# Performance work log

Hardware: AMD Instinct MI355X
Metric: run time of the kernel (lower is better)

The kernel has to match this reference:

```python
import jax, jax.numpy as jnp
import numpy as np

K = 2  # binary (k-ary) heap-layout tree: children of node j are K*j+1 .. K*j+K

def _levels(N):
    # level of node i in heap layout = floor(log2(i+1)); returns list of index arrays, root level first
    lev = np.floor(np.log2(np.arange(N) + 1)).astype(np.int64)
    depth = int(lev.max()) + 1
    return [np.where(lev == l)[0] for l in range(depth)]

def setup_inputs() -> dict:
    key = jax.random.key(0)
    ks = jax.random.split(key, 9)
    B, N, D = 512, 127, 300
    s = 0.05
    return {
        'x':     jax.random.normal(ks[0], (B, N, D), jnp.float32),
        'Wioux': jax.random.normal(ks[1], (D, 3 * D), jnp.float32) * s,
        'bioux': jax.random.normal(ks[2], (3 * D,), jnp.float32) * s,
        'Wiouh': jax.random.normal(ks[3], (D, 3 * D), jnp.float32) * s,
        'biouh': jax.random.normal(ks[4], (3 * D,), jnp.float32) * s,
        'Wfx':   jax.random.normal(ks[5], (D, D), jnp.float32) * s,
        'bfx':   jax.random.normal(ks[6], (D,), jnp.float32) * s,
        'Wfh':   jax.random.normal(ks[7], (D, D), jnp.float32) * s,
        'bfh':   jax.random.normal(ks[8], (D,), jnp.float32) * s,
    }

def reference(x, Wioux, bioux, Wiouh, biouh, Wfx, bfx, Wfh, bfh):
    # Child-Sum Tree-LSTM, level-synchronous (leaves -> root), batched over B trees.
    B, N, D = x.shape
    levels = _levels(N)
    H = jnp.zeros((B, N, D), x.dtype)
    C = jnp.zeros((B, N, D), x.dtype)
    for idx in reversed(levels):  # process deepest level first
        ch = idx[:, None] * K + 1 + np.arange(K)          # [n, K] child node ids (static)
        valid = jnp.asarray((ch < N), x.dtype)[None, :, :, None]  # [1,n,K,1]
        chc = np.minimum(ch, N - 1)
        ch_h = H[:, chc] * valid                           # [B,n,K,D]; padded children -> 0 (leaf case)
        ch_c = C[:, chc] * valid
        h_sum = ch_h.sum(axis=2)                           # child-sum of hidden states [B,n,D]
        xj = x[:, idx]                                     # [B,n,D]
        iou = xj @ Wioux + bioux + h_sum @ Wiouh + biouh   # [B,n,3D]
        i_g, o_g, u_g = jnp.split(iou, 3, axis=-1)
        i_g = jax.nn.sigmoid(i_g)
        o_g = jax.nn.sigmoid(o_g)
        u_g = jnp.tanh(u_g)
        fx = (xj @ Wfx + bfx)[:, :, None, :]               # broadcast over children
        f = jax.nn.sigmoid(jnp.einsum('bnkd,de->bnke', ch_h, Wfh) + bfh + fx)
        c = i_g * u_g + (f * ch_c).sum(axis=2)             # fc sum; padded ch_c==0
        h = o_g * jnp.tanh(c)
        H = H.at[:, idx].set(h)
        C = C.at[:, idx].set(c)
    return H  # per-node hidden states (contexts); root hidden = H[:, 0]
```

## Files before the change

### kernel.cpp

```cpp
#include <hip/hip_runtime.h>
#include <math.h>

#define DIM 300
#define NNODE 127
#define KP 320
#define BK 32
#define ASTR 40
#define MATSZ (KP*KP)

typedef __attribute__((ext_vector_type(8)))  short bf16x8;
typedef __attribute__((ext_vector_type(16))) float f32x16;

__device__ __forceinline__ unsigned short f2bf(float f){
    unsigned u = __float_as_uint(f);
    u += 0x7fffu + ((u >> 16) & 1u);
    return (unsigned short)(u >> 16);
}
__device__ __forceinline__ float sigf(float v){ return 1.0f/(1.0f+__expf(-v)); }
__device__ __forceinline__ float tanh_(float v){
    float t = __expf(-2.0f*fabsf(v));
    float r = (1.0f - t)/(1.0f + t);
    return v < 0.0f ? -r : r;
}

__global__ void prep_weights(const float* __restrict__ Wioux,
                             const float* __restrict__ Wiouh,
                             const float* __restrict__ Wfx,
                             const float* __restrict__ Wfh,
                             unsigned short* __restrict__ WT)
{
    int k = threadIdx.x;
    int n = blockIdx.x;
    int m = blockIdx.y;
    float v = 0.f;
    if (k < DIM && n < DIM){
        if (m < 3)       v = Wioux[k*(3*DIM) + m*DIM + n];
        else if (m < 6)  v = Wiouh[k*(3*DIM) + (m-3)*DIM + n];
        else if (m == 6) v = Wfx[k*DIM + n];
        else             v = Wfh[k*DIM + n];
    }
    WT[m*MATSZ + n*KP + k] = f2bf(v);
}

__global__ __launch_bounds__(256,2)
void leaf_mfma(const float* __restrict__ x,
               const float* __restrict__ bioux, const float* __restrict__ biouh,
               const unsigned short* __restrict__ WT,
               float* __restrict__ H, float* __restrict__ C)
{
    __shared__ __attribute__((aligned(16))) short lds[(1+3)*64*ASTR];
    short* As = lds;
    short* Bs = lds + 64*ASTR;

    const int t = threadIdx.x;
    const int lane = t & 63, wave = t >> 6;
    const int wm = wave >> 1, wn = wave & 1;
    const int lrow = lane & 31, half = lane >> 5;
    const int rowBase = blockIdx.x * 64;
    const int d0 = blockIdx.y * 64;

    const int sr = t >> 2, sseg = t & 3;
    const float* xrow;
    {
        int grow = rowBase + sr;
        int b = grow >> 6, j = 63 + (grow & 63);
        xrow = x + (b*NNODE + j)*DIM;
    }
    const int bm = t >> 5, bn = t & 31;

    f32x16 accI, accO, accU;
    #pragma unroll
    for (int i = 0; i < 16; i++){ accI[i]=0.f; accO[i]=0.f; accU[i]=0.f; }

    for (int k0 = 0; k0 < KP; k0 += BK){
        {
            int kk0 = k0 + sseg*8;
            bf16x8 px;
            if (kk0 + 8 <= DIM){
                float4 a0 = *(const float4*)(xrow + kk0);
                float4 a1 = *(const float4*)(xrow + kk0 + 4);
                px[0]=f2bf(a0.x); px[1]=f2bf(a0.y); px[2]=f2bf(a0.z); px[3]=f2bf(a0.w);
                px[4]=f2bf(a1.x); px[5]=f2bf(a1.y); px[6]=f2bf(a1.z); px[7]=f2bf(a1.w);
            } else {
                #pragma unroll
                for (int e = 0; e < 8; e++){
                    int k = kk0 + e;
                    px[e] = f2bf(k < DIM ? xrow[k] : 0.f);
                }
            }
            *(bf16x8*)(As + sr*ASTR + sseg*8) = px;
        }
        if (bm < 3){
            const unsigned short* wb = WT + bm*MATSZ + k0;
            #pragma unroll
            for (int h2 = 0; h2 < 2; h2++){
                int nn = bn + 32*h2;
                const unsigned short* src = wb + (d0 + nn)*KP;
                short* dst = Bs + bm*64*ASTR + nn*ASTR;
                *(bf16x8*)(dst)      = *(const bf16x8*)(src);
                *(bf16x8*)(dst + 8)  = *(const bf16x8*)(src + 8);
                *(bf16x8*)(dst + 16) = *(const bf16x8*)(src + 16);
                *(bf16x8*)(dst + 24) = *(const bf16x8*)(src + 24);
            }
        }
        __syncthreads();
        #pragma unroll
        for (int kk = 0; kk < 2; kk++){
            int ao = (wm*32 + lrow)*ASTR + kk*16 + half*8;
            bf16x8 ax = *(const bf16x8*)(As + ao);
            int bo = (wn*32 + lrow)*ASTR + kk*16 + half*8;
            bf16x8 b0 = *(const bf16x8*)(Bs + 0*64*ASTR + bo);
            bf16x8 b1 = *(const bf16x8*)(Bs + 1*64*ASTR + bo);
            bf16x8 b2 = *(const bf16x8*)(Bs + 2*64*ASTR + bo);
            accI = __builtin_amdgcn_mfma_f32_32x32x16_bf16(ax, b0, accI, 0, 0, 0);
            accO = __builtin_amdgcn_mfma_f32_32x32x16_bf16(ax, b1, accO, 0, 0, 0);
            accU = __builtin_amdgcn_mfma_f32_32x32x16_bf16(ax, b2, accU, 0, 0, 0);
        }
        __syncthreads();
    }
    int d = d0 + wn*32 + lrow;
    if (d < DIM){
        float bi  = bioux[d]       + biouh[d];
        float bo_ = bioux[DIM+d]   + biouh[DIM+d];
        float bu  = bioux[2*DIM+d] + biouh[2*DIM+d];
        #pragma unroll
        for (int q = 0; q < 16; q++){
            int grow = rowBase + wm*32 + (q&3) + 8*(q>>2) + 4*half;
            int b = grow >> 6, j = 63 + (grow & 63);
            int obase = (b*NNODE + j)*DIM + d;
            float iv = sigf (accI[q] + bi);
            float ov = sigf (accO[q] + bo_);
            float uv = tanh_(accU[q] + bu);
            float cv = iv*uv;
            C[obase] = cv;
            H[obase] = ov*tanh_(cv);
        }
    }
}

__global__ __launch_bounds__(256,2)
void level_mfma(const float* __restrict__ x,
                const float* __restrict__ bioux, const float* __restrict__ biouh,
                const float* __restrict__ bfx,   const float* __restrict__ bfh,
                const unsigned short* __restrict__ WT,
                float* __restrict__ H, float* __restrict__ C,
                int lo, int lshift)
{
    __shared__ __attribute__((aligned(16))) short lds[(4+8)*64*ASTR];
    short* As = lds;
    short* Bs = lds + 4*64*ASTR;

    const int t = threadIdx.x;
    const int lane = t & 63, wave = t >> 6;
    const int wm = wave >> 1, wn = wave & 1;
    const int lrow = lane & 31, half = lane >> 5;
    const int rowBase = blockIdx.x * 64;
    const int d0 = blockIdx.y * 64;
    const int nmask = (1 << lshift) - 1;

    const int sr = t >> 2, sseg = t & 3;
    const float *xrow, *h0row, *h1row;
    {
        int grow = rowBase + sr;
        int b = grow >> lshift, j = lo + (grow & nmask);
        xrow  = x + (b*NNODE + j)*DIM;
        h0row = H + (b*NNODE + 2*j+1)*DIM;
        h1row = H + (b*NNODE + 2*j+2)*DIM;
    }
    const int bm = t >> 5, bn = t & 31;

    f32x16 accI, accO, accU, accFx, accF0, accF1;
    #pragma unroll
    for (int i = 0; i < 16; i++){
        accI[i]=0.f; accO[i]=0.f; accU[i]=0.f;
        accFx[i]=0.f; accF0[i]=0.f; accF1[i]=0.f;
    }

    for (int k0 = 0; k0 < KP; k0 += BK){
        {
            int kk0 = k0 + sseg*8;
            int aoff = sr*ASTR + sseg*8;
            bf16x8 px;
            if (kk0 + 8 <= DIM){
                float4 a0 = *(const float4*)(xrow + kk0);
                float4 a1 = *(const float4*)(xrow + kk0 + 4);
                px[0]=f2bf(a0.x); px[1]=f2bf(a0.y); px[2]=f2bf(a0.z); px[3]=f2bf(a0.w);
                px[4]=f2bf(a1.x); px[5]=f2bf(a1.y); px[6]=f2bf(a1.z); px[7]=f2bf(a1.w);
            } else {
                #pragma unroll
                for (int e = 0; e < 8; e++){
                    int k = kk0 + e;
                    px[e] = f2bf(k < DIM ? xrow[k] : 0.f);
                }
            }
            *(bf16x8*)(As + aoff) = px;

            float h0v[8], h1v[8];
            if (kk0 + 8 <= DIM){
                float4 b0 = *(const float4*)(h0row + kk0);
                float4 b1 = *(const float4*)(h0row + kk0 + 4);
                float4 c0 = *(const float4*)(h1row + kk0);
                float4 c1 = *(const float4*)(h1row + kk0 + 4);
                h0v[0]=b0.x; h0v[1]=b0.y; h0v[2]=b0.z; h0v[3]=b0.w;
                h0v[4]=b1.x; h0v[5]=b1.y; h0v[6]=b1.z; h0v[7]=b1.w;
                h1v[0]=c0.x; h1v[1]=c0.y; h1v[2]=c0.z; h1v[3]=c0.w;
                h1v[4]=c1.x; h1v[5]=c1.y; h1v[6]=c1.z; h1v[7]=c1.w;
            } else {
                #pragma unroll
                for (int e = 0; e < 8; e++){
                    int k = kk0 + e;
                    bool ok = k < DIM;
                    h0v[e] = ok ? h0row[k] : 0.f;
                    h1v[e] = ok ? h1row[k] : 0.f;
                }
            }
            bf16x8 ph, p0, p1;
            #pragma unroll
            for (int e = 0; e < 8; e++){
                p0[e] = f2bf(h0v[e]);
                p1[e] = f2bf(h1v[e]);
                ph[e] = f2bf(h0v[e] + h1v[e]);
            }
            *(bf16x8*)(As + 1*64*ASTR + aoff) = ph;
            *(bf16x8*)(As + 2*64*ASTR + aoff) = p0;
            *(bf16x8*)(As + 3*64*ASTR + aoff) = p1;
        }
        {
            const unsigned short* wb = WT + bm*MATSZ + k0;
            #pragma unroll
            for (int h2 = 0; h2 < 2; h2++){
                int nn = bn + 32*h2;
                const unsigned short* src = wb + (d0 + nn)*KP;
                short* dst = Bs + bm*64*ASTR + nn*ASTR;
                *(bf16x8*)(dst)      = *(const bf16x8*)(src);
                *(bf16x8*)(dst + 8)  = *(const bf16x8*)(src + 8);
                *(bf16x8*)(dst + 16) = *(const bf16x8*)(src + 16);
                *(bf16x8*)(dst + 24) = *(const bf16x8*)(src + 24);
            }
        }
        __syncthreads();
        #pragma unroll
        for (int kk = 0; kk < 2; kk++){
            int ao = (wm*32 + lrow)*ASTR + kk*16 + half*8;
            bf16x8 ax = *(const bf16x8*)(As + 0*64*ASTR + ao);
            bf16x8 ah = *(const bf16x8*)(As + 1*64*ASTR + ao);
            bf16x8 a0 = *(const bf16x8*)(As + 2*64*ASTR + ao);
            bf16x8 a1 = *(const bf16x8*)(As + 3*64*ASTR + ao);
            int bo = (wn*32 + lrow)*ASTR + kk*16 + half*8;
            bf16x8 b0 = *(const bf16x8*)(Bs + 0*64*ASTR + bo);
            bf16x8 b1 = *(const bf16x8*)(Bs + 1*64*ASTR + bo);
            bf16x8 b2 = *(const bf16x8*)(Bs + 2*64*ASTR + bo);
            bf16x8 b3 = *(const bf16x8*)(Bs + 3*64*ASTR + bo);
            bf16x8 b4 = *(const bf16x8*)(Bs + 4*64*ASTR + bo);
            bf16x8 b5 = *(const bf16x8*)(Bs + 5*64*ASTR + bo);
            bf16x8 b6 = *(const bf16x8*)(Bs + 6*64*ASTR + bo);
            bf16x8 b7 = *(const bf16x8*)(Bs + 7*64*ASTR + bo);
            accI  = __builtin_amdgcn_mfma_f32_32x32x16_bf16(ax, b0, accI , 0, 0, 0);
            accI  = __builtin_amdgcn_mfma_f32_32x32x16_bf16(ah, b3, accI , 0, 0, 0);
            accO  = __builtin_amdgcn_mfma_f32_32x32x16_bf16(ax, b1, accO , 0, 0, 0);
            accO  = __builtin_amdgcn_mfma_f32_32x32x16_bf16(ah, b4, accO , 0, 0, 0);
            accU  = __builtin_amdgcn_mfma_f32_32x32x16_bf16(ax, b2, accU , 0, 0, 0);
            accU  = __builtin_amdgcn_mfma_f32_32x32x16_bf16(ah, b5, accU , 0, 0, 0);
            accFx = __builtin_amdgcn_mfma_f32_32x32x16_bf16(ax, b6, accFx, 0, 0, 0);
            accF0 = __builtin_amdgcn_mfma_f32_32x32x16_bf16(a0, b7, accF0, 0, 0, 0);
            accF1 = __builtin_amdgcn_mfma_f32_32x32x16_bf16(a1, b7, accF1, 0, 0, 0);
        }
        __syncthreads();
    }
    int d = d0 + wn*32 + lrow;
    if (d < DIM){
        float bi  = bioux[d]       + biouh[d];
        float bo_ = bioux[DIM+d]   + biouh[DIM+d];
        float bu  = bioux[2*DIM+d] + biouh[2*DIM+d];
        float bf_ = bfx[d] + bfh[d];
        #pragma unroll
        for (int q = 0; q < 16; q++){
            int grow = rowBase + wm*32 + (q&3) + 8*(q>>2) + 4*half;
            int b = grow >> lshift, j = lo + (grow & nmask);
            int obase = (b*NNODE + j)*DIM + d;
            int c0i = (b*NNODE + 2*j+1)*DIM + d;
            int c1i = (b*NNODE + 2*j+2)*DIM + d;
            float iv = sigf (accI[q] + bi);
            float ov = sigf (accO[q] + bo_);
            float uv = tanh_(accU[q] + bu);
            float f0 = sigf (accFx[q] + accF0[q] + bf_);
            float f1 = sigf (accFx[q] + accF1[q] + bf_);
            float cv = iv*uv + f0*C[c0i] + f1*C[c1i];
            C[obase] = cv;
            H[obase] = ov*tanh_(cv);
        }
    }
}

extern "C" void kernel_launch(void* const* d_in, const int* in_sizes, int n_in,
                              void* d_out, int out_size, void* d_ws, size_t ws_size,
                              hipStream_t stream) {
    const float* x     = (const float*)d_in[0];
    const float* Wioux = (const float*)d_in[1];
    const float* bioux = (const float*)d_in[2];
    const float* Wiouh = (const float*)d_in[3];
    const float* biouh = (const float*)d_in[4];
    const float* Wfx   = (const float*)d_in[5];
    const float* bfx   = (const float*)d_in[6];
    const float* Wfh   = (const float*)d_in[7];
    const float* bfh   = (const float*)d_in[8];
    float* H = (float*)d_out;
    float* C = (float*)d_ws;
    unsigned short* WT = (unsigned short*)((char*)d_ws + 78028800);

    prep_weights<<<dim3(KP, 8), KP, 0, stream>>>(Wioux, Wiouh, Wfx, Wfh, WT);
    leaf_mfma<<<dim3(512, 5), 256, 0, stream>>>(x, bioux, biouh, WT, H, C);
    for (int l = 5; l >= 0; l--){
        level_mfma<<<dim3(8 << l, 5), 256, 0, stream>>>(
            x, bioux, biouh, bfx, bfh, WT, H, C, (1 << l) - 1, l);
    }
}
```

Baseline: 532.0 us.

## Load weight fragments directly from global memory and drop LDS staging of B

```diff
diff --git a/kernel.cpp b/kernel.cpp
--- a/kernel.cpp
+++ b/kernel.cpp
@@ -6,7 +6,7 @@
 #define KP 320
 #define BK 32
 #define ASTR 40
-#define MATSZ (KP*KP)
+#define WROW (8*KP)
 
 typedef __attribute__((ext_vector_type(8)))  short bf16x8;
 typedef __attribute__((ext_vector_type(16))) float f32x16;
@@ -39,18 +39,16 @@
         else if (m == 6) v = Wfx[k*DIM + n];
         else             v = Wfh[k*DIM + n];
     }
-    WT[m*MATSZ + n*KP + k] = f2bf(v);
-}
-
-__global__ __launch_bounds__(256,2)
+    WT[n*WROW + m*KP + k] = f2bf(v);
+}
+
+__global__ __launch_bounds__(256,4)
 void leaf_mfma(const float* __restrict__ x,
                const float* __restrict__ bioux, const float* __restrict__ biouh,
                const unsigned short* __restrict__ WT,
                float* __restrict__ H, float* __restrict__ C)
 {
-    __shared__ __attribute__((aligned(16))) short lds[(1+3)*64*ASTR];
-    short* As = lds;
-    short* Bs = lds + 64*ASTR;
+    __shared__ __attribute__((aligned(16))) short As[64*ASTR];
 
     const int t = threadIdx.x;
     const int lane = t & 63, wave = t >> 6;
@@ -66,7 +64,7 @@
         int b = grow >> 6, j = 63 + (grow & 63);
         xrow = x + (b*NNODE + j)*DIM;
     }
-    const int bm = t >> 5, bn = t & 31;
+    const unsigned short* wrow = WT + (size_t)(d0 + wn*32 + lrow)*WROW;
 
     f32x16 accI, accO, accU;
     #pragma unroll
@@ -90,28 +88,15 @@
             }
             *(bf16x8*)(As + sr*ASTR + sseg*8) = px;
         }
-        if (bm < 3){
-            const unsigned short* wb = WT + bm*MATSZ + k0;
-            #pragma unroll
-            for (int h2 = 0; h2 < 2; h2++){
-                int nn = bn + 32*h2;
-                const unsigned short* src = wb + (d0 + nn)*KP;
-                short* dst = Bs + bm*64*ASTR + nn*ASTR;
-                *(bf16x8*)(dst)      = *(const bf16x8*)(src);
-                *(bf16x8*)(dst + 8)  = *(const bf16x8*)(src + 8);
-                *(bf16x8*)(dst + 16) = *(const bf16x8*)(src + 16);
-                *(bf16x8*)(dst + 24) = *(const bf16x8*)(src + 24);
-            }
-        }
         __syncthreads();
         #pragma unroll
         for (int kk = 0; kk < 2; kk++){
             int ao = (wm*32 + lrow)*ASTR + kk*16 + half*8;
             bf16x8 ax = *(const bf16x8*)(As + ao);
-            int bo = (wn*32 + lrow)*ASTR + kk*16 + half*8;
-            bf16x8 b0 = *(const bf16x8*)(Bs + 0*64*ASTR + bo);
-            bf16x8 b1 = *(const bf16x8*)(Bs + 1*64*ASTR + bo);
-            bf16x8 b2 = *(const bf16x8*)(Bs + 2*64*ASTR + bo);
+            const unsigned short* wk = wrow + k0 + kk*16 + half*8;
+            bf16x8 b0 = *(const bf16x8*)(wk);
+            bf16x8 b1 = *(const bf16x8*)(wk + KP);
+            bf16x8 b2 = *(const bf16x8*)(wk + 2*KP);
             accI = __builtin_amdgcn_mfma_f32_32x32x16_bf16(ax, b0, accI, 0, 0, 0);
             accO = __builtin_amdgcn_mfma_f32_32x32x16_bf16(ax, b1, accO, 0, 0, 0);
             accU = __builtin_amdgcn_mfma_f32_32x32x16_bf16(ax, b2, accU, 0, 0, 0);
@@ -138,7 +123,7 @@
     }
 }
 
-__global__ __launch_bounds__(256,2)
+__global__ __launch_bounds__(256,3)
 void level_mfma(const float* __restrict__ x,
                 const float* __restrict__ bioux, const float* __restrict__ biouh,
                 const float* __restrict__ bfx,   const float* __restrict__ bfh,
@@ -146,9 +131,7 @@
                 float* __restrict__ H, float* __restrict__ C,
                 int lo, int lshift)
 {
-    __shared__ __attribute__((aligned(16))) short lds[(4+8)*64*ASTR];
-    short* As = lds;
-    short* Bs = lds + 4*64*ASTR;
+    __shared__ __attribute__((aligned(16))) short As[4*64*ASTR];
 
     const int t = threadIdx.x;
     const int lane = t & 63, wave = t >> 6;
@@ -167,15 +150,15 @@
         h0row = H + (b*NNODE + 2*j+1)*DIM;
         h1row = H + (b*NNODE + 2*j+2)*DIM;
     }
-    const int bm = t >> 5, bn = t & 31;
-
-    f32x16 accI, accO, accU, accFx, accF0, accF1;
+    const unsigned short* wrow = WT + (size_t)(d0 + wn*32 + lrow)*WROW;
+
+    f32x16 accI, accO, accU, accF0, accF1;
     #pragma unroll
     for (int i = 0; i < 16; i++){
-        accI[i]=0.f; accO[i]=0.f; accU[i]=0.f;
-        accFx[i]=0.f; accF0[i]=0.f; accF1[i]=0.f;
-    }
-
+        accI[i]=0.f; accO[i]=0.f; accU[i]=0.f; accF0[i]=0.f; accF1[i]=0.f;
+    }
+
+    #pragma unroll 1
     for (int k0 = 0; k0 < KP; k0 += BK){
         {
             int kk0 = k0 + sseg*8;
@@ -225,43 +208,31 @@
             *(bf16x8*)(As + 2*64*ASTR + aoff) = p0;
             *(bf16x8*)(As + 3*64*ASTR + aoff) = p1;
         }
-        {
-            const unsigned short* wb = WT + bm*MATSZ + k0;
-            #pragma unroll
-            for (int h2 = 0; h2 < 2; h2++){
-                int nn = bn + 32*h2;
-                const unsigned short* src = wb + (d0 + nn)*KP;
-                short* dst = Bs + bm*64*ASTR + nn*ASTR;
-                *(bf16x8*)(dst)      = *(const bf16x8*)(src);
-                *(bf16x8*)(dst + 8)  = *(const bf16x8*)(src + 8);
-                *(bf16x8*)(dst + 16) = *(const bf16x8*)(src + 16);
-                *(bf16x8*)(dst + 24) = *(const bf16x8*)(src + 24);
-            }
-        }
         __syncthreads();
         #pragma unroll
         for (int kk = 0; kk < 2; kk++){
             int ao = (wm*32 + lrow)*ASTR + kk*16 + half*8;
-            bf16x8 ax = *(const bf16x8*)(As + 0*64*ASTR + ao);
+            const unsigned short* wk = wrow + k0 + kk*16 + half*8;
+            bf16x8 ax = *(const bf16x8*)(As + ao);
+            bf16x8 b0 = *(const bf16x8*)(wk);
+            bf16x8 b1 = *(const bf16x8*)(wk + KP);
+            bf16x8 b2 = *(const bf16x8*)(wk + 2*KP);
+            bf16x8 b6 = *(const bf16x8*)(wk + 6*KP);
+            accI  = __builtin_amdgcn_mfma_f32_32x32x16_bf16(ax, b0, accI , 0, 0, 0);
+            accO  = __builtin_amdgcn_mfma_f32_32x32x16_bf16(ax, b1, accO , 0, 0, 0);
+            accU  = __builtin_amdgcn_mfma_f32_32x32x16_bf16(ax, b2, accU , 0, 0, 0);
+            accF0 = __builtin_amdgcn_mfma_f32_32x32x16_bf16(ax, b6, accF0, 0, 0, 0);
+            accF1 = __builtin_amdgcn_mfma_f32_32x32x16_bf16(ax, b6, accF1, 0, 0, 0);
             bf16x8 ah = *(const bf16x8*)(As + 1*64*ASTR + ao);
+            bf16x8 b3 = *(const bf16x8*)(wk + 3*KP);
+            bf16x8 b4 = *(const bf16x8*)(wk + 4*KP);
+            bf16x8 b5 = *(const bf16x8*)(wk + 5*KP);
+            accI  = __builtin_amdgcn_mfma_f32_32x32x16_bf16(ah, b3, accI , 0, 0, 0);
+            accO  = __builtin_amdgcn_mfma_f32_32x32x16_bf16(ah, b4, accO , 0, 0, 0);
+            accU  = __builtin_amdgcn_mfma_f32_32x32x16_bf16(ah, b5, accU , 0, 0, 0);
             bf16x8 a0 = *(const bf16x8*)(As + 2*64*ASTR + ao);
             bf16x8 a1 = *(const bf16x8*)(As + 3*64*ASTR + ao);
-            int bo = (wn*32 + lrow)*ASTR + kk*16 + half*8;
-            bf16x8 b0 = *(const bf16x8*)(Bs + 0*64*ASTR + bo);
-            bf16x8 b1 = *(const bf16x8*)(Bs + 1*64*ASTR + bo);
-            bf16x8 b2 = *(const bf16x8*)(Bs + 2*64*ASTR + bo);
-            bf16x8 b3 = *(const bf16x8*)(Bs + 3*64*ASTR + bo);
-            bf16x8 b4 = *(const bf16x8*)(Bs + 4*64*ASTR + bo);
-            bf16x8 b5 = *(const bf16x8*)(Bs + 5*64*ASTR + bo);
-            bf16x8 b6 = *(const bf16x8*)(Bs + 6*64*ASTR + bo);
-            bf16x8 b7 = *(const bf16x8*)(Bs + 7*64*ASTR + bo);
-            accI  = __builtin_amdgcn_mfma_f32_32x32x16_bf16(ax, b0, accI , 0, 0, 0);
-            accI  = __builtin_amdgcn_mfma_f32_32x32x16_bf16(ah, b3, accI , 0, 0, 0);
-            accO  = __builtin_amdgcn_mfma_f32_32x32x16_bf16(ax, b1, accO , 0, 0, 0);
-            accO  = __builtin_amdgcn_mfma_f32_32x32x16_bf16(ah, b4, accO , 0, 0, 0);
-            accU  = __builtin_amdgcn_mfma_f32_32x32x16_bf16(ax, b2, accU , 0, 0, 0);
-            accU  = __builtin_amdgcn_mfma_f32_32x32x16_bf16(ah, b5, accU , 0, 0, 0);
-            accFx = __builtin_amdgcn_mfma_f32_32x32x16_bf16(ax, b6, accFx, 0, 0, 0);
+            bf16x8 b7 = *(const bf16x8*)(wk + 7*KP);
             accF0 = __builtin_amdgcn_mfma_f32_32x32x16_bf16(a0, b7, accF0, 0, 0, 0);
             accF1 = __builtin_amdgcn_mfma_f32_32x32x16_bf16(a1, b7, accF1, 0, 0, 0);
         }
@@ -283,8 +254,8 @@
             float iv = sigf (accI[q] + bi);
             float ov = sigf (accO[q] + bo_);
             float uv = tanh_(accU[q] + bu);
-            float f0 = sigf (accFx[q] + accF0[q] + bf_);
-            float f1 = sigf (accFx[q] + accF1[q] + bf_);
+            float f0 = sigf (accF0[q] + bf_);
+            float f1 = sigf (accF1[q] + bf_);
             float cv = iv*uv + f0*C[c0i] + f1*C[c1i];
             C[obase] = cv;
             H[obase] = ov*tanh_(cv);
```

New measurement: 661.1 us. 24.3% more time.

## Prefetch next K-tile into registers while MFMAs consume current LDS tile

Applied to the files above, without the earlier changes.

```diff
diff --git a/kernel.cpp b/kernel.cpp
--- a/kernel.cpp
+++ b/kernel.cpp
@@ -10,6 +10,8 @@
 
 typedef __attribute__((ext_vector_type(8)))  short bf16x8;
 typedef __attribute__((ext_vector_type(16))) float f32x16;
+
+#define BARRIER() asm volatile("s_waitcnt lgkmcnt(0)\n\ts_barrier" ::: "memory")
 
 __device__ __forceinline__ unsigned short f2bf(float f){
     unsigned u = __float_as_uint(f);
@@ -42,7 +44,7 @@
     WT[m*MATSZ + n*KP + k] = f2bf(v);
 }
 
-__global__ __launch_bounds__(256,2)
+__global__ __launch_bounds__(256,3)
 void leaf_mfma(const float* __restrict__ x,
                const float* __restrict__ bioux, const float* __restrict__ biouh,
                const unsigned short* __restrict__ WT,
@@ -72,38 +74,58 @@
     #pragma unroll
     for (int i = 0; i < 16; i++){ accI[i]=0.f; accO[i]=0.f; accU[i]=0.f; }
 
-    for (int k0 = 0; k0 < KP; k0 += BK){
-        {
-            int kk0 = k0 + sseg*8;
-            bf16x8 px;
-            if (kk0 + 8 <= DIM){
-                float4 a0 = *(const float4*)(xrow + kk0);
-                float4 a1 = *(const float4*)(xrow + kk0 + 4);
-                px[0]=f2bf(a0.x); px[1]=f2bf(a0.y); px[2]=f2bf(a0.z); px[3]=f2bf(a0.w);
-                px[4]=f2bf(a1.x); px[5]=f2bf(a1.y); px[6]=f2bf(a1.z); px[7]=f2bf(a1.w);
-            } else {
-                #pragma unroll
-                for (int e = 0; e < 8; e++){
-                    int k = kk0 + e;
-                    px[e] = f2bf(k < DIM ? xrow[k] : 0.f);
-                }
+    float xa[8];
+    bf16x8 wstage[2][4];
+
+    auto LOAD = [&](int k0){
+        int kk0 = k0 + sseg*8;
+        if (kk0 + 8 <= DIM){
+            float4 a0 = *(const float4*)(xrow + kk0);
+            float4 a1 = *(const float4*)(xrow + kk0 + 4);
+            xa[0]=a0.x; xa[1]=a0.y; xa[2]=a0.z; xa[3]=a0.w;
+            xa[4]=a1.x; xa[5]=a1.y; xa[6]=a1.z; xa[7]=a1.w;
+        } else {
+            #pragma unroll
+            for (int e = 0; e < 8; e++){
+                int k = kk0 + e;
+                xa[e] = (k < DIM) ? xrow[k] : 0.f;
             }
-            *(bf16x8*)(As + sr*ASTR + sseg*8) = px;
         }
         if (bm < 3){
             const unsigned short* wb = WT + bm*MATSZ + k0;
             #pragma unroll
             for (int h2 = 0; h2 < 2; h2++){
-                int nn = bn + 32*h2;
-                const unsigned short* src = wb + (d0 + nn)*KP;
-                short* dst = Bs + bm*64*ASTR + nn*ASTR;
-                *(bf16x8*)(dst)      = *(const bf16x8*)(src);
-                *(bf16x8*)(dst + 8)  = *(const bf16x8*)(src + 8);
-                *(bf16x8*)(dst + 16) = *(const bf16x8*)(src + 16);
-                *(bf16x8*)(dst + 24) = *(const bf16x8*)(src + 24);
+                const unsigned short* src = wb + (size_t)(d0 + bn + 32*h2)*KP;
+                wstage[h2][0] = *(const bf16x8*)(src);
+                wstage[h2][1] = *(const bf16x8*)(src + 8);
+                wstage[h2][2] = *(const bf16x8*)(src + 16);
+                wstage[h2][3] = *(const bf16x8*)(src + 24);
             }
         }
-        __syncthreads();
+    };
+    auto STORE = [&](){
+        bf16x8 px;
+        #pragma unroll
+        for (int e = 0; e < 8; e++) px[e] = f2bf(xa[e]);
+        *(bf16x8*)(As + sr*ASTR + sseg*8) = px;
+        if (bm < 3){
+            #pragma unroll
+            for (int h2 = 0; h2 < 2; h2++){
+                short* dst = Bs + bm*64*ASTR + (bn + 32*h2)*ASTR;
+                *(bf16x8*)(dst)      = wstage[h2][0];
+                *(bf16x8*)(dst + 8)  = wstage[h2][1];
+                *(bf16x8*)(dst + 16) = wstage[h2][2];
+                *(bf16x8*)(dst + 24) = wstage[h2][3];
+            }
+        }
+    };
+
+    LOAD(0);
+    #pragma unroll 1
+    for (int ks = 0; ks < KP/BK; ks++){
+        STORE();
+        BARRIER();
+        if (ks + 1 < KP/BK) LOAD((ks+1)*BK);
         #pragma unroll
         for (int kk = 0; kk < 2; kk++){
             int ao = (wm*32 + lrow)*ASTR + kk*16 + half*8;
@@ -116,7 +138,7 @@
             accO = __builtin_amdgcn_mfma_f32_32x32x16_bf16(ax, b1, accO, 0, 0, 0);
             accU = __builtin_amdgcn_mfma_f32_32x32x16_bf16(ax, b2, accU, 0, 0, 0);
         }
-        __syncthreads();
+        BARRIER();
     }
     int d = d0 + wn*32 + lrow;
     if (d < DIM){
@@ -176,69 +198,74 @@
         accFx[i]=0.f; accF0[i]=0.f; accF1[i]=0.f;
     }
 
-    for (int k0 = 0; k0 < KP; k0 += BK){
-        {
-            int kk0 = k0 + sseg*8;
-            int aoff = sr*ASTR + sseg*8;
-            bf16x8 px;
-            if (kk0 + 8 <= DIM){
-                float4 a0 = *(const float4*)(xrow + kk0);
-                float4 a1 = *(const float4*)(xrow + kk0 + 4);
-                px[0]=f2bf(a0.x); px[1]=f2bf(a0.y); px[2]=f2bf(a0.z); px[3]=f2bf(a0.w);
-                px[4]=f2bf(a1.x); px[5]=f2bf(a1.y); px[6]=f2bf(a1.z); px[7]=f2bf(a1.w);
-            } else {
-                #pragma unroll
-                for (int e = 0; e < 8; e++){
-                    int k = kk0 + e;
-                    px[e] = f2bf(k < DIM ? xrow[k] : 0.f);
-                }
-            }
-            *(bf16x8*)(As + aoff) = px;
-
-            float h0v[8], h1v[8];
-            if (kk0 + 8 <= DIM){
-                float4 b0 = *(const float4*)(h0row + kk0);
-                float4 b1 = *(const float4*)(h0row + kk0 + 4);
-                float4 c0 = *(const float4*)(h1row + kk0);
-                float4 c1 = *(const float4*)(h1row + kk0 + 4);
-                h0v[0]=b0.x; h0v[1]=b0.y; h0v[2]=b0.z; h0v[3]=b0.w;
-                h0v[4]=b1.x; h0v[5]=b1.y; h0v[6]=b1.z; h0v[7]=b1.w;
-                h1v[0]=c0.x; h1v[1]=c0.y; h1v[2]=c0.z; h1v[3]=c0.w;
-                h1v[4]=c1.x; h1v[5]=c1.y; h1v[6]=c1.z; h1v[7]=c1.w;
-            } else {
-                #pragma unroll
-                for (int e = 0; e < 8; e++){
-                    int k = kk0 + e;
-                    bool ok = k < DIM;
-                    h0v[e] = ok ? h0row[k] : 0.f;
-                    h1v[e] = ok ? h1row[k] : 0.f;
-                }
-            }
-            bf16x8 ph, p0, p1;
+    float xa[8], h0v[8], h1v[8];
+    bf16x8 wstage[2][4];
+
+    auto LOAD = [&](int k0){
+        int kk0 = k0 + sseg*8;
+        if (kk0 + 8 <= DIM){
+            float4 a0 = *(const float4*)(xrow + kk0);
+            float4 a1 = *(const float4*)(xrow + kk0 + 4);
+            float4 b0 = *(const float4*)(h0row + kk0);
+            float4 b1 = *(const float4*)(h0row + kk0 + 4);
+            float4 c0 = *(const float4*)(h1row + kk0);
+            float4 c1 = *(const float4*)(h1row + kk0 + 4);
+            xa[0]=a0.x;  xa[1]=a0.y;  xa[2]=a0.z;  xa[3]=a0.w;
+            xa[4]=a1.x;  xa[5]=a1.y;  xa[6]=a1.z;  xa[7]=a1.w;
+            h0v[0]=b0.x; h0v[1]=b0.y; h0v[2]=b0.z; h0v[3]=b0.w;
+            h0v[4]=b1.x; h0v[5]=b1.y; h0v[6]=b1.z; h0v[7]=b1.w;
+            h1v[0]=c0.x; h1v[1]=c0.y; h1v[2]=c0.z; h1v[3]=c0.w;
+            h1v[4]=c1.x; h1v[5]=c1.y; h1v[6]=c1.z; h1v[7]=c1.w;
+        } else {
             #pragma unroll
             for (int e = 0; e < 8; e++){
-                p0[e] = f2bf(h0v[e]);
-                p1[e] = f2bf(h1v[e]);
-                ph[e] = f2bf(h0v[e] + h1v[e]);
+                int k = kk0 + e;
+                bool ok = k < DIM;
+                xa[e]  = ok ? xrow[k]  : 0.f;
+                h0v[e] = ok ? h0row[k] : 0.f;
+                h1v[e] = ok ? h1row[k] : 0.f;
             }
-            *(bf16x8*)(As + 1*64*ASTR + aoff) = ph;
-            *(bf16x8*)(As + 2*64*ASTR + aoff) = p0;
-            *(bf16x8*)(As + 3*64*ASTR + aoff) = p1;
-        }
-        {
-            const unsigned short* wb = WT + bm*MATSZ + k0;
-            #pragma unroll
-            for (int h2 = 0; h2 < 2; h2++){
-                int nn = bn + 32*h2;
-                const unsigned short* src = wb + (d0 + nn)*KP;
-                short* dst = Bs + bm*64*ASTR + nn*ASTR;
-                *(bf16x8*)(dst)      = *(const bf16x8*)(src);
-                *(bf16x8*)(dst + 8)  = *(const bf16x8*)(src + 8);
-                *(bf16x8*)(dst + 16) = *(const bf16x8*)(src + 16);
-                *(bf16x8*)(dst + 24) = *(const bf16x8*)(src + 24);
-            }
-        }
-        __syncthreads();
+        }
+        const unsigned short* wb = WT + bm*MATSZ + k0;
+        #pragma unroll
+        for (int h2 = 0; h2 < 2; h2++){
+            const unsigned short* src = wb + (size_t)(d0 + bn + 32*h2)*KP;
+            wstage[h2][0] = *(const bf16x8*)(src);
+            wstage[h2][1] = *(const bf16x8*)(src + 8);
+            wstage[h2][2] = *(const bf16x8*)(src + 16);
+            wstage[h2][3] = *(const bf16x8*)(src + 24);
+        }
+    };
+    auto STORE = [&](){
+        int aoff = sr*ASTR + sseg*8;
+        bf16x8 px, ph, p0, p1;
+        #pragma unroll
+        for (int e = 0; e < 8; e++){
+            px[e] = f2bf(xa[e]);
+            p0[e] = f2bf(h0v[e]);
+            p1[e] = f2bf(h1v[e]);
+            ph[e] = f2bf(h0v[e] + h1v[e]);
+        }
+        *(bf16x8*)(As + aoff) = px;
+        *(bf16x8*)(As + 1*64*ASTR + aoff) = ph;
+        *(bf16x8*)(As + 2*64*ASTR + aoff) = p0;
+        *(bf16x8*)(As + 3*64*ASTR + aoff) = p1;
+        #pragma unroll
+        for (int h2 = 0; h2 < 2; h2++){
+            short* dst = Bs + bm*64*ASTR + (bn + 32*h2)*ASTR;
+            *(bf16x8*)(dst)      = wstage[h2][0];
+            *(bf16x8*)(dst + 8)  = wstage[h2][1];
+            *(bf16x8*)(dst + 16) = wstage[h2][2];
+            *(bf16x8*)(dst + 24) = wstage[h2][3];
+        }
+    };
+
+    LOAD(0);
+    #pragma unroll 1
+    for (int ks = 0; ks < KP/BK; ks++){
+        STORE();
+        BARRIER();
+        if (ks + 1 < KP/BK) LOAD((ks+1)*BK);
         #pragma unroll
         for (int kk = 0; kk < 2; kk++){
             int ao = (wm*32 + lrow)*ASTR + kk*16 + half*8;
@@ -265,7 +292,7 @@
             accF0 = __builtin_amdgcn_mfma_f32_32x32x16_bf16(a0, b7, accF0, 0, 0, 0);
             accF1 = __builtin_amdgcn_mfma_f32_32x32x16_bf16(a1, b7, accF1, 0, 0, 0);
         }
-        __syncthreads();
+        BARRIER();
     }
     int d = d0 + wn*32 + lrow;
     if (d < DIM){
```

Result: no change. 539.1 us (+1.3%).
